# Performance work log

Hardware: AMD Instinct MI355X
Metric: run time of the kernel (lower is better)

The kernel has to match this reference:

```python
import jax, jax.numpy as jnp
import numpy as np

IN_DIM = 128
HIDDEN = 128


def setup_inputs() -> dict:
    key = jax.random.key(0)
    k1, k2, k3, k4, k5 = jax.random.split(key, 5)
    bound_ih = 1.0 / np.sqrt(IN_DIM)
    bound_hh = 1.0 / np.sqrt(HIDDEN)
    return {
        "x": jax.random.normal(k1, (256, 2048, IN_DIM), dtype=jnp.float32),
        "W_ih": jax.random.uniform(k2, (HIDDEN, IN_DIM), minval=-bound_ih, maxval=bound_ih, dtype=jnp.float32),
        "b_ih": jax.random.uniform(k3, (HIDDEN,), minval=-bound_ih, maxval=bound_ih, dtype=jnp.float32),
        "W_hh": jax.random.uniform(k4, (HIDDEN, HIDDEN), minval=-bound_hh, maxval=bound_hh, dtype=jnp.float32),
        "b_hh": jax.random.uniform(k5, (HIDDEN,), minval=-bound_hh, maxval=bound_hh, dtype=jnp.float32),
    }


def reference(x, W_ih, b_ih, W_hh, b_hh):
    B, S, _ = x.shape
    # Precompute input projection for all timesteps in one big GEMM: [B,S,H]
    xw = jnp.einsum("bsi,hi->bsh", x, W_ih) + b_ih
    h0 = jnp.zeros((B, W_hh.shape[0]), dtype=x.dtype)

    def step(h, xw_t):
        h_new = jnp.tanh(xw_t + h @ W_hh.T + b_hh)
        return h_new, None

    # scan over time axis: move S to leading dim
    h_final, _ = jax.lax.scan(step, h0, jnp.swapaxes(xw, 0, 1))
    return h_final
```

## Files before the change

### kernel.cpp

```cpp
#include <hip/hip_runtime.h>


#define BATCH 256
#define SEQ   2048
#define HID   128
#define CH    16
#define NCHUNK (SEQ / CH)

template <int CTRL>
__device__ __forceinline__ float dpp_movf(float x) {
    return __int_as_float(__builtin_amdgcn_mov_dpp(__float_as_int(x), CTRL, 0xF, 0xF, true));
}

__device__ __forceinline__ float tanh_fast(float x) {
    x = fminf(fmaxf(x, -12.0f), 12.0f);
    float e = __expf(2.0f * x);
    return 1.0f - __fdividef(2.0f, e + 1.0f);
}

__global__ __launch_bounds__(256, 1) void rnn_scan_kernel(
    const float* __restrict__ x,
    const float* __restrict__ Wih,
    const float* __restrict__ bih,
    const float* __restrict__ Whh,
    const float* __restrict__ bhh,
    float* __restrict__ out)
{
    const int b = blockIdx.x;
    const int t = threadIdx.x;
    const int g = t >> 4;
    const int c = t & 15;
    const int colbase = c << 3;
    const int rowbase = g << 3;

    __shared__ __align__(16) float xbuf[2][CH * HID];
    __shared__ __align__(16) float hbuf[2][192];

    float4 wi[8][2], wh[8][2];
#pragma unroll
    for (int r = 0; r < 8; ++r) {
        const float* pi = Wih + (rowbase + r) * HID + colbase;
        const float* ph = Whh + (rowbase + r) * HID + colbase;
        wi[r][0] = *(const float4*)(pi);
        wi[r][1] = *(const float4*)(pi + 4);
        wh[r][0] = *(const float4*)(ph);
        wh[r][1] = *(const float4*)(ph + 4);
    }

    const int m = c & 3;
    const int o = ((m & 1) << 2) | (m & 2);
    const int row0 = rowbase + o;
    const float bias0 = bih[row0] + bhh[row0];
    const float bias1 = bih[row0 + 1] + bhh[row0 + 1];
    const int hw = row0 + (g << 2);

    const float* xsrc = x + (size_t)b * (SEQ * HID);

    {
        const float4* gp = (const float4*)xsrc;
        float4 p0 = gp[t];
        float4 p1 = gp[256 + t];
        float4* lb = (float4*)&xbuf[0][0];
        lb[t] = p0;
        lb[256 + t] = p1;
    }
    if (t < 192) hbuf[0][t] = 0.0f;
    __syncthreads();

    int cur = 0;
    for (int chn = 0; chn < NCHUNK; ++chn) {
        float4 q0, q1;
        const bool pf = (chn + 1 < NCHUNK);
        if (pf) {
            const float4* gp = (const float4*)(xsrc + (size_t)(chn + 1) * (CH * HID));
            q0 = gp[t];
            q1 = gp[256 + t];
        }
        const float* xb = &xbuf[chn & 1][0];
#pragma unroll 1
        for (int s = 0; s < CH; ++s) {
            const float* xr = xb + s * HID + colbase;
            const float* hr = &hbuf[cur][12 * c];
            float4 xv0 = *(const float4*)(xr);
            float4 xv1 = *(const float4*)(xr + 4);
            float4 hv0 = *(const float4*)(hr);
            float4 hv1 = *(const float4*)(hr + 4);

            float a[8];
#pragma unroll
            for (int r = 0; r < 8; ++r) {
                float acc;
                acc = wi[r][0].x * xv0.x;
                acc = fmaf(wi[r][0].y, xv0.y, acc);
                acc = fmaf(wi[r][0].z, xv0.z, acc);
                acc = fmaf(wi[r][0].w, xv0.w, acc);
                acc = fmaf(wi[r][1].x, xv1.x, acc);
                acc = fmaf(wi[r][1].y, xv1.y, acc);
                acc = fmaf(wi[r][1].z, xv1.z, acc);
                acc = fmaf(wi[r][1].w, xv1.w, acc);
                acc = fmaf(wh[r][0].x, hv0.x, acc);
                acc = fmaf(wh[r][0].y, hv0.y, acc);
                acc = fmaf(wh[r][0].z, hv0.z, acc);
                acc = fmaf(wh[r][0].w, hv0.w, acc);
                acc = fmaf(wh[r][1].x, hv1.x, acc);
                acc = fmaf(wh[r][1].y, hv1.y, acc);
                acc = fmaf(wh[r][1].z, hv1.z, acc);
                acc = fmaf(wh[r][1].w, hv1.w, acc);
                a[r] = acc;
            }

            const bool b0 = (c & 1) != 0;
            const bool b1 = (c & 2) != 0;
            float k0 = b0 ? a[4] : a[0], g0 = b0 ? a[0] : a[4];
            float k1 = b0 ? a[5] : a[1], g1 = b0 ? a[1] : a[5];
            float k2 = b0 ? a[6] : a[2], g2 = b0 ? a[2] : a[6];
            float k3 = b0 ? a[7] : a[3], g3 = b0 ? a[3] : a[7];
            float t0 = k0 + dpp_movf<0xB1>(g0);
            float t1 = k1 + dpp_movf<0xB1>(g1);
            float t2 = k2 + dpp_movf<0xB1>(g2);
            float t3 = k3 + dpp_movf<0xB1>(g3);
            float k4 = b1 ? t2 : t0, g4 = b1 ? t0 : t2;
            float k5 = b1 ? t3 : t1, g5 = b1 ? t1 : t3;
            float u0 = k4 + dpp_movf<0x4E>(g4);
            float u1 = k5 + dpp_movf<0x4E>(g5);
            u0 += dpp_movf<0x124>(u0);
            u1 += dpp_movf<0x124>(u1);
            u0 += dpp_movf<0x128>(u0);
            u1 += dpp_movf<0x128>(u1);

            float h0 = tanh_fast(u0 + bias0);
            float h1 = tanh_fast(u1 + bias1);
            if (c < 4) {
                *(float2*)&hbuf[cur ^ 1][hw] = make_float2(h0, h1);
            }

            if (s == CH - 1 && pf) {
                float4* lb = (float4*)&xbuf[(chn + 1) & 1][0];
                lb[t] = q0;
                lb[256 + t] = q1;
            }
            __syncthreads();
            cur ^= 1;
        }
    }
    if (t < HID) out[(size_t)b * HID + t] = hbuf[cur][t + ((t >> 3) << 2)];
}

extern "C" void kernel_launch(void* const* d_in, const int* in_sizes, int n_in,
                              void* d_out, int out_size, void* d_ws, size_t ws_size,
                              hipStream_t stream) {
    const float* x   = (const float*)d_in[0];
    const float* Wih = (const float*)d_in[1];
    const float* bih = (const float*)d_in[2];
    const float* Whh = (const float*)d_in[3];
    const float* bhh = (const float*)d_in[4];
    float* out = (float*)d_out;

    rnn_scan_kernel<<<BATCH, 256, 0, stream>>>(x, Wih, bih, Whh, bhh, out);
}
```

Measured before the change: 1.313 ms.

## Pad x smem layout, permute weight rows to drop selects, pin weights

```diff
diff --git a/kernel.cpp b/kernel.cpp
--- a/kernel.cpp
+++ b/kernel.cpp
@@ -6,6 +6,7 @@
 #define HID   128
 #define CH    16
 #define NCHUNK (SEQ / CH)
+#define XPAD  192
 
 template <int CTRL>
 __device__ __forceinline__ float dpp_movf(float x) {
@@ -18,7 +19,11 @@
     return 1.0f - __fdividef(2.0f, e + 1.0f);
 }
 
-__global__ __launch_bounds__(256, 1) void rnn_scan_kernel(
+#define PIN4(v) asm volatile("" : "+v"(v.x), "+v"(v.y), "+v"(v.z), "+v"(v.w))
+
+__global__ __launch_bounds__(256)
+__attribute__((amdgpu_waves_per_eu(1)))
+void rnn_scan_kernel(
     const float* __restrict__ x,
     const float* __restrict__ Wih,
     const float* __restrict__ bih,
@@ -31,40 +36,42 @@
     const int g = t >> 4;
     const int c = t & 15;
     const int colbase = c << 3;
-    const int rowbase = g << 3;
+    const int xoff = 12 * c;
 
-    __shared__ __align__(16) float xbuf[2][CH * HID];
-    __shared__ __align__(16) float hbuf[2][192];
+    __shared__ __align__(16) float xbuf[2][CH * XPAD];
+    __shared__ __align__(16) float hbuf[2][XPAD];
 
+    const int p = ((c & 1) << 2) | (c & 2);
     float4 wi[8][2], wh[8][2];
 #pragma unroll
     for (int r = 0; r < 8; ++r) {
-        const float* pi = Wih + (rowbase + r) * HID + colbase;
-        const float* ph = Whh + (rowbase + r) * HID + colbase;
+        const int row = (g << 3) + (r ^ p);
+        const float* pi = Wih + row * HID + colbase;
+        const float* ph = Whh + row * HID + colbase;
         wi[r][0] = *(const float4*)(pi);
         wi[r][1] = *(const float4*)(pi + 4);
         wh[r][0] = *(const float4*)(ph);
         wh[r][1] = *(const float4*)(ph + 4);
     }
 
-    const int m = c & 3;
-    const int o = ((m & 1) << 2) | (m & 2);
-    const int row0 = rowbase + o;
+    const int row0 = (g << 3) + p;
     const float bias0 = bih[row0] + bhh[row0];
     const float bias1 = bih[row0 + 1] + bhh[row0 + 1];
-    const int hw = row0 + (g << 2);
+    const int hw = 12 * g + p;
+
+    const int m0 = t & 31;
+    const int dst0 = XPAD * (t >> 5) + 12 * (m0 >> 1) + ((m0 & 1) << 2);
+    const int dst1 = dst0 + XPAD * 8;
 
     const float* xsrc = x + (size_t)b * (SEQ * HID);
 
     {
         const float4* gp = (const float4*)xsrc;
-        float4 p0 = gp[t];
-        float4 p1 = gp[256 + t];
-        float4* lb = (float4*)&xbuf[0][0];
-        lb[t] = p0;
-        lb[256 + t] = p1;
+        float4 p0 = gp[t], p1 = gp[256 + t];
+        *(float4*)&xbuf[0][dst0] = p0;
+        *(float4*)&xbuf[0][dst1] = p1;
     }
-    if (t < 192) hbuf[0][t] = 0.0f;
+    if (t < XPAD) hbuf[0][t] = 0.0f;
     __syncthreads();
 
     int cur = 0;
@@ -79,12 +86,17 @@
         const float* xb = &xbuf[chn & 1][0];
 #pragma unroll 1
         for (int s = 0; s < CH; ++s) {
-            const float* xr = xb + s * HID + colbase;
-            const float* hr = &hbuf[cur][12 * c];
+#pragma unroll
+            for (int r = 0; r < 8; ++r) {
+                PIN4(wi[r][0]); PIN4(wi[r][1]);
+                PIN4(wh[r][0]); PIN4(wh[r][1]);
+            }
+            const float* hr = &hbuf[cur][xoff];
+            float4 hv0 = *(const float4*)(hr);
+            float4 hv1 = *(const float4*)(hr + 4);
+            const float* xr = xb + s * XPAD + xoff;
             float4 xv0 = *(const float4*)(xr);
             float4 xv1 = *(const float4*)(xr + 4);
-            float4 hv0 = *(const float4*)(hr);
-            float4 hv1 = *(const float4*)(hr + 4);
 
             float a[8];
 #pragma unroll
@@ -98,6 +110,11 @@
                 acc = fmaf(wi[r][1].y, xv1.y, acc);
                 acc = fmaf(wi[r][1].z, xv1.z, acc);
                 acc = fmaf(wi[r][1].w, xv1.w, acc);
+                a[r] = acc;
+            }
+#pragma unroll
+            for (int r = 0; r < 8; ++r) {
+                float acc = a[r];
                 acc = fmaf(wh[r][0].x, hv0.x, acc);
                 acc = fmaf(wh[r][0].y, hv0.y, acc);
                 acc = fmaf(wh[r][0].z, hv0.z, acc);
@@ -109,35 +126,27 @@
                 a[r] = acc;
             }
 
-            const bool b0 = (c & 1) != 0;
-            const bool b1 = (c & 2) != 0;
-            float k0 = b0 ? a[4] : a[0], g0 = b0 ? a[0] : a[4];
-            float k1 = b0 ? a[5] : a[1], g1 = b0 ? a[1] : a[5];
-            float k2 = b0 ? a[6] : a[2], g2 = b0 ? a[2] : a[6];
-            float k3 = b0 ? a[7] : a[3], g3 = b0 ? a[3] : a[7];
-            float t0 = k0 + dpp_movf<0xB1>(g0);
-            float t1 = k1 + dpp_movf<0xB1>(g1);
-            float t2 = k2 + dpp_movf<0xB1>(g2);
-            float t3 = k3 + dpp_movf<0xB1>(g3);
-            float k4 = b1 ? t2 : t0, g4 = b1 ? t0 : t2;
-            float k5 = b1 ? t3 : t1, g5 = b1 ? t1 : t3;
-            float u0 = k4 + dpp_movf<0x4E>(g4);
-            float u1 = k5 + dpp_movf<0x4E>(g5);
+            float t0 = a[0] + dpp_movf<0xB1>(a[4]);
+            float t1 = a[1] + dpp_movf<0xB1>(a[5]);
+            float t2 = a[2] + dpp_movf<0xB1>(a[6]);
+            float t3 = a[3] + dpp_movf<0xB1>(a[7]);
+            float u0 = t0 + dpp_movf<0x4E>(t2);
+            float u1 = t1 + dpp_movf<0x4E>(t3);
             u0 += dpp_movf<0x124>(u0);
             u1 += dpp_movf<0x124>(u1);
             u0 += dpp_movf<0x128>(u0);
             u1 += dpp_movf<0x128>(u1);
 
-            float h0 = tanh_fast(u0 + bias0);
-            float h1 = tanh_fast(u1 + bias1);
             if (c < 4) {
+                float h0 = tanh_fast(u0 + bias0);
+                float h1 = tanh_fast(u1 + bias1);
                 *(float2*)&hbuf[cur ^ 1][hw] = make_float2(h0, h1);
             }
 
             if (s == CH - 1 && pf) {
-                float4* lb = (float4*)&xbuf[(chn + 1) & 1][0];
-                lb[t] = q0;
-                lb[256 + t] = q1;
+                float* nb = &xbuf[(chn + 1) & 1][0];
+                *(float4*)&nb[dst0] = q0;
+                *(float4*)&nb[dst1] = q1;
             }
             __syncthreads();
             cur ^= 1;
```

New measurement: 1.449 ms. +10.3%, slower.
